# Kernel optimization log

Hardware: AMD Instinct MI355X
Metric: run time of the kernel (lower is better)

The kernel has to match this reference:

```python
import jax, jax.numpy as jnp
import numpy as np

# WAGE-style quantizer (NeuroSim training path): round to 2^(b-1) levels, clip to (-1+1/S, 1-1/S),
# straight-through estimator for gradients.

def wage_q(x, bits=8):
    S = 2.0 ** (bits - 1)
    q = jnp.clip(jnp.round(x * S) / S, -1.0 + 1.0 / S, 1.0 - 1.0 / S)
    return x + jax.lax.stop_gradient(q - x)


def qconv(x, w, stride, pad, wl_w=8, wl_a=8):
    wq = wage_q(w, wl_w)
    y = jax.lax.conv_general_dilated(
        x, wq, window_strides=(stride, stride),
        padding=[(pad, pad), (pad, pad)],
        dimension_numbers=('NCHW', 'OIHW', 'NCHW'))
    return wage_q(y, wl_a)


def pad_hw(x, p):
    return jnp.pad(x, ((0, 0), (0, 0), (p, p), (p, p)))


def crop_like(x, tgt):
    return x[:, :, :tgt.shape[2], :tgt.shape[3]]


WEIGHT_SHAPES = {
    'w1': (64, 4, 3, 3), 'w2': (128, 64, 3, 3), 'w3': (256, 128, 3, 3), 'w4': (512, 256, 3, 3),
    'wr11': (512, 512, 3, 3), 'wr12': (512, 512, 3, 3), 'wr21': (512, 512, 3, 3), 'wr22': (512, 512, 3, 3),
    'wd3': (128, 512, 4, 4), 'wd2': (64, 416, 4, 4), 'wd1': (4, 224, 4, 4),
    'wu43': (32, 512, 4, 4), 'wu32': (32, 416, 4, 4), 'wu21': (32, 224, 4, 4), 'wu10': (32, 100, 4, 4),
    'wfc': (1, 32),
}


def setup_inputs() -> dict:
    key = jax.random.key(0)
    keys = jax.random.split(key, len(WEIGHT_SHAPES) + 1)
    inp = {'x': jax.random.normal(keys[0], (8, 4, 256, 256), dtype=jnp.float32)}
    for i, (name, shp) in enumerate(WEIGHT_SHAPES.items()):
        fan_in = int(np.prod(shp[1:]))
        inp[name] = jax.random.normal(keys[i + 1], shp, dtype=jnp.float32) / np.sqrt(fan_in)
    return inp


def reference(x, w1, w2, w3, w4, wr11, wr12, wr21, wr22,
              wd3, wd2, wd1, wu43, wu32, wu21, wu10, wfc):
    c1 = qconv(x, w1, 2, 1)        # [B,64,128,128]
    c2 = qconv(c1, w2, 2, 1)       # [B,128,64,64]
    c3 = qconv(c2, w3, 2, 1)       # [B,256,32,32]
    c4 = qconv(c3, w4, 2, 1)       # [B,512,16,16]
    r11 = qconv(c4, wr11, 1, 1)
    r12 = (1.0 - qconv(r11, wr12, 1, 1)) * c4
    r21 = qconv(r12, wr21, 1, 1)
    r22 = (1.0 - qconv(r21, wr22, 1, 1)) * r12
    r22p = pad_hw(r22, 8)                                   # [B,512,32,32]
    flow4_up = crop_like(qconv(r22p, wu43, 1, 2), c3)       # [B,32,32,32]
    d3 = crop_like(qconv(r22p, wd3, 1, 2), c3)              # [B,128,32,32]
    cat3 = pad_hw(jnp.concatenate([c3, d3, flow4_up], 1), 16)  # [B,416,64,64]
    flow3_up = crop_like(qconv(cat3, wu32, 1, 2), c2)
    d2 = crop_like(qconv(cat3, wd2, 1, 2), c2)
    cat2 = pad_hw(jnp.concatenate([c2, d2, flow3_up], 1), 32)  # [B,224,128,128]
    flow2_up = crop_like(qconv(cat2, wu21, 1, 2), c1)
    d1 = crop_like(qconv(cat2, wd1, 1, 2), c1)
    cat1 = pad_hw(jnp.concatenate([c1, d1, flow2_up], 1), 64)  # [B,100,256,256]
    u10 = qconv(cat1, wu10, 1, 2)                              # [B,32,257,257]
    feat = jnp.max(u10, axis=(2, 3))                           # AdaptiveMaxPool2d((1,1))
    out = wage_q(feat @ wage_q(wfc, 8).T, 8)                   # QLinear 32->1
    return out
```

## Files before the change

### kernel.cpp

```cpp
#include <hip/hip_runtime.h>

#define DEV __device__ __forceinline__

typedef __attribute__((ext_vector_type(4))) int i32x4;

DEV int wqi(float y) {
    int q = (int)rintf(y * 128.0f);
    return q < -127 ? -127 : (q > 127 ? 127 : q);
}
DEV unsigned encf(float f) { unsigned u = __float_as_uint(f); return (u & 0x80000000u) ? ~u : (u | 0x80000000u); }
DEV float decf(unsigned u) { return (u & 0x80000000u) ? __uint_as_float(u ^ 0x80000000u) : __uint_as_float(~u); }
DEV float wq8f(float x) {
    float q = rintf(x * 128.0f) * 0.0078125f;
    return fminf(fmaxf(q, -0.9921875f), 0.9921875f);
}

#define GLOAD16(g, l) __builtin_amdgcn_global_load_lds( \
    (const __attribute__((address_space(1))) void*)(g), \
    (__attribute__((address_space(3))) void*)(l), 16, 0, 0)

struct PackDesc {
    const float* w0; const float* w1; uint4* dst;
    int OC0, OC1, CinW, K, noct, nch64u, ndup, gsz;
};
struct PackArgs { PackDesc d[11]; int bofs[12]; };

__global__ void __launch_bounds__(256) k_packall(PackArgs a) {
    __shared__ unsigned char sb[16 * (64 * 16 + 4)];
    const int b = blockIdx.x;
    int i = 0;
    #pragma unroll
    for (int j = 1; j < 11; ++j) if (b >= a.bofs[j]) i = j;
    const PackDesc D = a.d[i];
    const int b2 = b - a.bofs[i];
    const int oct = b2 % D.noct;
    const int ch64u = b2 / D.noct;
    const int K2 = D.K * D.K;
    const int NCHT = D.nch64u * D.ndup;
    const int row_elems = 64 * K2;
    const int SSTR = row_elems + 4;
    const int QR = row_elems / 4;
    const int NQ = 16 * QR;
    const int cin0 = ch64u * 64;
    const int tid = threadIdx.x;
    const int og = oct / D.gsz, ol = oct % D.gsz;

    for (int q = tid; q < NQ; q += 256) {
        const int r = q / QR, j = q - r * QR;
        const int oc = oct * 16 + r;
        const float* src = nullptr; int oci = 0;
        if (oc < D.OC0) { src = D.w0; oci = oc; }
        else if (oc < D.OC0 + D.OC1) { src = D.w1; oci = oc - D.OC0; }
        const int e0 = j * 4;
        float v[4] = {0.f, 0.f, 0.f, 0.f};
        if (src != nullptr) {
            const float* p = src + ((size_t)oci * D.CinW + cin0) * K2 + e0;
            const int cin_last = cin0 + (e0 + 3) / K2;
            if (cin_last < D.CinW) {
                const float4 f4 = *(const float4*)p;
                v[0] = f4.x; v[1] = f4.y; v[2] = f4.z; v[3] = f4.w;
            } else {
                #pragma unroll
                for (int e = 0; e < 4; ++e) {
                    const int cin = cin0 + (e0 + e) / K2;
                    if (cin < D.CinW) v[e] = p[e];
                }
            }
        }
        unsigned pk = 0;
        #pragma unroll
        for (int e = 0; e < 4; ++e) pk |= ((unsigned)(wqi(v[e]) & 255)) << (e * 8);
        *(unsigned*)&sb[r * SSTR + e0] = pk;
    }
    __syncthreads();

    const int outN = K2 * 64;
    for (int idx = tid; idx < outN; idx += 256) {
        const int kpos = idx >> 6, lane = idx & 63;
        const int l15 = lane & 15, g = lane >> 4;
        unsigned wd[4] = {0u, 0u, 0u, 0u};
        #pragma unroll
        for (int e = 0; e < 16; ++e) {
            const unsigned bval = sb[l15 * SSTR + (g * 16 + e) * K2 + kpos];
            wd[e >> 2] |= bval << ((e & 3) * 8);
        }
        uint4 u; u.x = wd[0]; u.y = wd[1]; u.z = wd[2]; u.w = wd[3];
        for (int d = 0; d < D.ndup; ++d) {
            const int ch64 = ch64u + d * D.nch64u;
            D.dst[((size_t)((og * NCHT + ch64) * K2 + kpos) * D.gsz + ol) * 64 + lane] = u;
        }
    }
}

__global__ void __launch_bounds__(256) k_conv1(const float* __restrict__ x, const float* __restrict__ w1,
                                               signed char* __restrict__ cat1) {
    __shared__ float sw2[36][64];
    __shared__ float sin_[4][17][17];
    const int tid = threadIdx.x;
    const int n = blockIdx.y;
    const int oh0 = (blockIdx.x >> 4) * 8, ow0 = (blockIdx.x & 15) * 8;
    for (int i = tid; i < 2304; i += 256) sw2[i % 36][i / 36] = wq8f(w1[i]);
    const int ih0 = oh0 * 2 - 1, iw0 = ow0 * 2 - 1;
    for (int i = tid; i < 4 * 289; i += 256) {
        const int c = i / 289, rem = i % 289, r = rem / 17, cc = rem % 17;
        const int ih = ih0 + r, iw = iw0 + cc;
        float v = 0.f;
        if ((unsigned)ih < 256u && (unsigned)iw < 256u) v = x[((size_t)(n * 4 + c) * 256 + ih) * 256 + iw];
        sin_[c][r][cc] = v;
    }
    __syncthreads();
    const int sp = tid & 63, ocg = tid >> 6;
    const int oh = sp >> 3, ow = sp & 7;
    float acc[16];
    #pragma unroll
    for (int j = 0; j < 16; ++j) acc[j] = 0.f;
    #pragma unroll
    for (int c = 0; c < 4; ++c)
    #pragma unroll
    for (int kh = 0; kh < 3; ++kh)
    #pragma unroll
    for (int kw = 0; kw < 3; ++kw) {
        const float v = sin_[c][oh * 2 + kh][ow * 2 + kw];
        const float4* wp4 = (const float4*)&sw2[c * 9 + kh * 3 + kw][ocg * 16];
        #pragma unroll
        for (int q = 0; q < 4; ++q) {
            const float4 wv = wp4[q];
            acc[q * 4 + 0] = fmaf(v, wv.x, acc[q * 4 + 0]);
            acc[q * 4 + 1] = fmaf(v, wv.y, acc[q * 4 + 1]);
            acc[q * 4 + 2] = fmaf(v, wv.z, acc[q * 4 + 2]);
            acc[q * 4 + 3] = fmaf(v, wv.w, acc[q * 4 + 3]);
        }
    }
    const size_t pix = ((size_t)(n * 128) + oh0 + oh) * 128 + ow0 + ow;
    unsigned wd[4] = {0u, 0u, 0u, 0u};
    #pragma unroll
    for (int j = 0; j < 16; ++j)
        wd[j >> 2] |= ((unsigned)(wqi(acc[j]) & 255)) << ((j & 3) * 8);
    uint4 u; u.x = wd[0]; u.y = wd[1]; u.z = wd[2]; u.w = wd[3];
    *(uint4*)(cat1 + pix * 112 + ocg * 16) = u;
}

__global__ void k_init(unsigned* __restrict__ feat, uint4* __restrict__ zbuf) {
    feat[threadIdx.x] = encf(-2.0f);
    if (threadIdx.x < 64) { uint4 z; z.x = z.y = z.z = z.w = 0u; zbuf[threadIdx.x] = z; }
}

__global__ void k_fc(const unsigned* __restrict__ feat, const float* __restrict__ wfc,
                     float* __restrict__ out) {
    int n = threadIdx.x;
    if (n < 8) {
        float s = 0.f;
        for (int c = 0; c < 32; ++c) s += decf(feat[n * 32 + c]) * wq8f(wfc[c]);
        out[n] = wq8f(s);
    }
}

template<int CMODE>
__global__ void __launch_bounds__(256) k_comb(const int* __restrict__ ps, int D, int G,
                                              int NP, int OC, double inv,
                                              signed char* __restrict__ dst, int dstr, int dch,
                                              const void* __restrict__ res, int rstr,
                                              signed char* __restrict__ dhl, int dhlstr,
                                              short* __restrict__ dj) {
    const int t = blockIdx.x * 256 + threadIdx.x;
    const int opc = OC / 4;
    const int total = NP * opc;
    if (t >= total) return;
    const int pix = t / opc, oc0 = (t - pix * opc) * 4;
    const size_t base = (size_t)pix * OC + oc0;
    const size_t NPOC = (size_t)NP * OC;
    long v[4] = {0, 0, 0, 0};
    int sidx = 0;
    for (int d = 0; d < D; ++d) {
        long s0 = 0, s1 = 0, s2 = 0, s3 = 0;
        for (int g = 0; g < G; ++g, ++sidx) {
            const int4 p = *(const int4*)(ps + sidx * NPOC + base);
            s0 += p.x; s1 += p.y; s2 += p.z; s3 += p.w;
        }
        v[0] = v[0] * 256 + s0; v[1] = v[1] * 256 + s1;
        v[2] = v[2] * 256 + s2; v[3] = v[3] * 256 + s3;
    }
    if constexpr (CMODE == 0) {
        unsigned pk = 0;
        #pragma unroll
        for (int j = 0; j < 4; ++j)
            pk |= (unsigned)(wqi((float)((double)v[j] * inv)) & 255) << (j * 8);
        *(unsigned*)(dst + (size_t)pix * dstr + dch + oc0) = pk;
    } else {
        #pragma unroll
        for (int j = 0; j < 4; ++j) {
            const int qi = wqi((float)((double)v[j] * inv));
            const int oc = oc0 + j;
            if constexpr (CMODE == 1) {
                const int rv = (int)((const signed char*)res)[(size_t)pix * rstr + oc];
                const int jj = (128 - qi) * rv;
                const int d0 = ((jj + 128) & 255) - 128;
                const int t1 = (jj - d0) >> 8;
                dhl[(size_t)pix * dhlstr + oc] = (signed char)t1;
                dhl[(size_t)pix * dhlstr + 512 + oc] = (signed char)d0;
                dj[(size_t)pix * 512 + oc] = (short)jj;
            } else {
                const int rv = (int)((const short*)res)[(size_t)pix * rstr + oc];
                const int jj = (128 - qi) * rv;
                const int d0 = ((jj + 128) & 255) - 128;
                const int t1 = (jj - d0) >> 8;
                const int d1 = ((t1 + 128) & 255) - 128;
                const int d2 = (t1 - d1) >> 8;
                dhl[(size_t)pix * dhlstr + oc] = (signed char)d2;
                dhl[(size_t)pix * dhlstr + 512 + oc] = (signed char)d1;
                dhl[(size_t)pix * dhlstr + 1024 + oc] = (signed char)d0;
            }
        }
    }
}

template<int K, int STR, int WM, int WN, int BN, int CHQ, int NBUF, int MODE>
__global__ void __launch_bounds__(256) k_mconv(
    const signed char* __restrict__ s0, int Ctot, int st0,
    int S, int padeff,
    const uint4* __restrict__ wqp, int nchtot,
    signed char* __restrict__ dst, int dstr, int dch,
    unsigned* __restrict__ feat, int* __restrict__ ps,
    const signed char* __restrict__ zbuf,
    int OCv, int OH, int OW, int TILES_W, int nch,
    int NT, int NOCG, int swzq, int ORD)
{
    constexpr int TH = WM * 4;
    constexpr int RH = (TH - 1) * STR + K, RW = 7 * STR + K;
    constexpr int UNITS = CHQ / 16;
    constexpr int UPPS = UNITS + 1;
    constexpr int NKC = CHQ / 64;
    constexpr int K2 = K * K;
    constexpr int NUS = RH * RW * UPPS;
    constexpr int ROUNDS = (NUS + 255) / 256;
    constexpr int NUPS = ROUNDS * 256;
    constexpr int AHEAD = NBUF - 1;
    __shared__ uint4 lds[NBUF * NUPS];
    __shared__ int sred[4][2][16];

    const int tid = threadIdx.x, lane = tid & 63, w = tid >> 6;
    const int wm = w % WM, wn = w / WM;
    const int l15 = lane & 15, g = lane >> 4;

    const int b = blockIdx.x;
    const int work = (b & 7) * swzq + (b >> 3);
    int tile, n, ocg, slice;
    if (ORD == 0) {
        ocg = work % NOCG; const int t2 = work / NOCG;
        tile = t2 % NT; const int t3 = t2 / NT;
        n = t3 & 7; slice = t3 >> 3;
    } else {
        tile = work % NT; const int t2 = work / NT;
        n = t2 & 7; const int t3 = t2 >> 3;
        ocg = t3 % NOCG; slice = t3 / NOCG;
    }
    const int cin_off = slice * nch * CHQ;
    const int group = ocg * WN + wn;

    const int tileh = tile / TILES_W, tilew = tile % TILES_W;
    const int oh0 = tileh * TH, ow0 = tilew * 8;
    const int ih0 = oh0 * STR - padeff, iw0 = ow0 * STR - padeff;
    const int blk_oct0 = ocg * (WN * BN);

    int pixb[2];
    #pragma unroll
    for (int am = 0; am < 2; ++am) {
        const int sp = wm * 32 + am * 16 + l15;
        pixb[am] = ((sp >> 3) * STR) * RW + (sp & 7) * STR;
    }

    int climit[ROUNDS];
    const signed char* gpb[ROUNDS];
    #pragma unroll
    for (int rd = 0; rd < ROUNDS; ++rd) {
        const int d = rd * 256 + tid;
        int cl = -1;
        const signed char* gb = zbuf;
        if (d < NUS) {
            const int pix = d / UPPS;
            const int u = d - pix * UPPS;
            const int r = pix / RW, c = pix - r * RW;
            const int ih = ih0 + r, iw = iw0 + c;
            if (u < UNITS && (unsigned)ih < (unsigned)S && (unsigned)iw < (unsigned)S) {
                cl = Ctot - cin_off - u * 16;
                gb = s0 + (((size_t)n * S + ih) * S + iw) * st0 + cin_off + u * 16;
            }
        }
        climit[rd] = cl; gpb[rd] = gb;
    }

    i32x4 acc[2][BN];
    #pragma unroll
    for (int am = 0; am < 2; ++am)
        #pragma unroll
        for (int bn = 0; bn < BN; ++bn) acc[am][bn] = (i32x4){0, 0, 0, 0};

    auto issue = [&](int ch, int buf) {
        uint4* lb = &lds[buf * NUPS];
        const int chv = ch * CHQ;
        #pragma unroll
        for (int rd = 0; rd < ROUNDS; ++rd) {
            const signed char* gp = (chv < climit[rd]) ? (gpb[rd] + chv) : zbuf;
            GLOAD16(gp, lb + rd * 256 + (tid & ~63));
        }
    };

    #pragma unroll
    for (int i = 0; i < AHEAD; ++i) if (i < nch) issue(i, i % NBUF);

    for (int ch = 0; ch < nch; ++ch) {
        if (ch + AHEAD < nch) issue(ch + AHEAD, (ch + AHEAD) % NBUF);
        const int infl = (nch - 1 - ch < AHEAD) ? nch - 1 - ch : AHEAD;
        if (infl >= 2)      __builtin_amdgcn_s_waitcnt(0xF70 | (2 * ROUNDS));
        else if (infl == 1) __builtin_amdgcn_s_waitcnt(0xF70 | ROUNDS);
        else                __builtin_amdgcn_s_waitcnt(0xF70);
        __builtin_amdgcn_s_barrier();
        __builtin_amdgcn_sched_barrier(0);
        const int bufo = (ch % NBUF) * NUPS;
        const int pb0 = bufo + pixb[0] * UPPS + g;
        const int pb1 = bufo + pixb[1] * UPPS + g;
        const uint4* wrow = wqp + ((size_t)(group * nchtot + (slice * nch + ch) * NKC) * K2 * BN) * 64 + lane;
        #pragma unroll
        for (int kpos = 0; kpos < K2; ++kpos) {
            const int kh = kpos / K, kw = kpos % K;
            const int po = (kh * RW + kw) * UPPS;
            #pragma unroll
            for (int kc = 0; kc < NKC; ++kc) {
                i32x4 bfr[BN];
                #pragma unroll
                for (int bn = 0; bn < BN; ++bn) {
                    union { uint4 u; i32x4 v; } bu;
                    bu.u = wrow[(kc * K2 * BN + kpos * BN + bn) * 64];
                    bfr[bn] = bu.v;
                }
                union { uint4 u; i32x4 v; } a0, a1;
                a0.u = lds[pb0 + po + kc * 4];
                a1.u = lds[pb1 + po + kc * 4];
                #pragma unroll
                for (int bn = 0; bn < BN; ++bn) {
                    acc[0][bn] = __builtin_amdgcn_mfma_i32_16x16x64_i8(a0.v, bfr[bn], acc[0][bn], 0, 0, 0);
                    acc[1][bn] = __builtin_amdgcn_mfma_i32_16x16x64_i8(a1.v, bfr[bn], acc[1][bn], 0, 0, 0);
                }
            }
        }
        __builtin_amdgcn_sched_barrier(0);
        __builtin_amdgcn_s_barrier();
    }

    if constexpr (MODE == 2) {
        #pragma unroll
        for (int bn = 0; bn < BN; ++bn) {
            int m = (int)0x80000000;
            #pragma unroll
            for (int am = 0; am < 2; ++am)
                #pragma unroll
                for (int rg = 0; rg < 4; ++rg) {
                    const int sp = wm * 32 + am * 16 + g * 4 + rg;
                    const int oh = oh0 + (sp >> 3), ow = ow0 + (sp & 7);
                    const int v = acc[am][bn][rg];
                    if (oh < OH && ow < OW && v > m) m = v;
                }
            int o = __shfl_xor(m, 16); if (o > m) m = o;
            o = __shfl_xor(m, 32); if (o > m) m = o;
            if (lane < 16) sred[w][bn][l15] = m;
        }
        __syncthreads();
        if (tid < BN * 16) {
            const int bn = tid >> 4, l = tid & 15;
            int mm = sred[0][bn][l];
            #pragma unroll
            for (int i = 1; i < WM * WN; ++i) { const int o = sred[i][bn][l]; if (o > mm) mm = o; }
            const float y = (float)mm * (1.f / 16384.f);
            const float v = (float)wqi(y) * 0.0078125f;
            atomicMax(&feat[n * 32 + (blk_oct0 + bn) * 16 + l], encf(v));
        }
    } else if constexpr (MODE == 3) {
        #pragma unroll
        for (int am = 0; am < 2; ++am)
        #pragma unroll
        for (int bn = 0; bn < BN; ++bn)
        #pragma unroll
        for (int rg = 0; rg < 4; ++rg) {
            const int sp = wm * 32 + am * 16 + g * 4 + rg;
            const int oh = oh0 + (sp >> 3), ow = ow0 + (sp & 7);
            const int oc = (blk_oct0 + wn * BN + bn) * 16 + l15;
            if (oh < OH && ow < OW && oc < OCv) {
                ps[(((size_t)slice * 8 + n) * OH * OW + (size_t)oh * OW + ow) * OCv + oc] = acc[am][bn][rg];
            }
        }
    } else {
        #pragma unroll
        for (int am = 0; am < 2; ++am)
        #pragma unroll
        for (int bn = 0; bn < BN; ++bn)
        #pragma unroll
        for (int rg = 0; rg < 4; ++rg) {
            const int sp = wm * 32 + am * 16 + g * 4 + rg;
            const int oh = oh0 + (sp >> 3), ow = ow0 + (sp & 7);
            const int oc = (blk_oct0 + wn * BN + bn) * 16 + l15;
            if (oh < OH && ow < OW && oc < OCv) {
                const size_t pixo = (size_t)(n * OH + oh) * OW + ow;
                const float y = (float)acc[am][bn][rg] * (1.f / 16384.f);
                dst[pixo * dstr + dch + oc] = (signed char)wqi(y);
            }
        }
    }
}

extern "C" void kernel_launch(void* const* d_in, const int* in_sizes, int n_in,
                              void* d_out, int out_size, void* d_ws, size_t ws_size,
                              hipStream_t stream)
{
    (void)in_sizes; (void)n_in; (void)out_size; (void)ws_size;
    const float* x = (const float*)d_in[0];
    const float* wfc = (const float*)d_in[16];
    float* out = (float*)d_out;

    char* ws = (char*)d_ws;
    size_t off = 0;
    auto alloc = [&](size_t bytes) { char* p = ws + off; off += (bytes + 255) & ~(size_t)255; return p; };

    struct PH { int i0, OC0, i1, OC1, CinW, K, noct, nch64u, ndup, gsz; };
    static const PH ph[11] = {
        {2, 128, -1, 0,  64, 3,  8, 1, 1, 2},
        {3, 256, -1, 0, 128, 3, 16, 2, 1, 2},
        {4, 512, -1, 0, 256, 3, 32, 4, 1, 2},
        {5, 512, -1, 0, 512, 3, 32, 8, 1, 2},
        {6, 512, -1, 0, 512, 3, 32, 8, 1, 2},
        {7, 512, -1, 0, 512, 3, 32, 8, 2, 2},
        {8, 512, -1, 0, 512, 3, 32, 8, 1, 2},
        {9, 128, 12, 32, 512, 4, 10, 8, 3, 2},
        {10, 64, 13, 32, 416, 4,  6, 7, 1, 2},
        {11,  4, 14, 32, 224, 4,  3, 4, 1, 3},
        {15, 32, -1, 0, 100, 4,  2, 2, 1, 2}};

    PackArgs pa;
    int bacc = 0;
    uint4* wp[11];
    for (int i = 0; i < 11; ++i) {
        const int nch64 = ph[i].nch64u * ph[i].ndup;
        const int nel = nch64 * ph[i].K * ph[i].K * ph[i].noct * 64;
        wp[i] = (uint4*)alloc((size_t)nel * 16);
        pa.d[i].w0 = (const float*)d_in[ph[i].i0];
        pa.d[i].w1 = (ph[i].i1 >= 0) ? (const float*)d_in[ph[i].i1] : nullptr;
        pa.d[i].dst = wp[i];
        pa.d[i].OC0 = ph[i].OC0; pa.d[i].OC1 = ph[i].OC1;
        pa.d[i].CinW = ph[i].CinW; pa.d[i].K = ph[i].K; pa.d[i].noct = ph[i].noct;
        pa.d[i].nch64u = ph[i].nch64u; pa.d[i].ndup = ph[i].ndup;
        pa.d[i].gsz = ph[i].gsz;
        pa.bofs[i] = bacc;
        bacc += ph[i].noct * ph[i].nch64u;
    }
    pa.bofs[11] = bacc;

    signed char* cat1b = (signed char*)alloc((size_t)8*128*128*112);
    signed char* cat2b = (signed char*)alloc((size_t)8*64*64*224);
    signed char* cat3b = (signed char*)alloc((size_t)8*32*32*416);
    signed char* c4b   = (signed char*)alloc((size_t)8*16*16*512);
    signed char* r11b  = (signed char*)alloc((size_t)8*16*16*512);
    signed char* r12d  = (signed char*)alloc((size_t)8*16*16*1024);
    short*       r12j  = (short*)alloc((size_t)8*16*16*512 * 2);
    signed char* r22d  = (signed char*)alloc((size_t)8*16*16*1536);
    int*         psum  = (int*)alloc((size_t)4*8*16*16*512 * 4);
    unsigned*    featb = (unsigned*)alloc(256 * 4);
    uint4*       zbuf  = (uint4*)alloc(1024);

    k_packall<<<dim3((unsigned)bacc), dim3(256), 0, stream>>>(pa);
    k_init<<<dim3(1), dim3(256), 0, stream>>>(featb, zbuf);
    k_conv1<<<dim3(256, 8), dim3(256), 0, stream>>>(x, (const float*)d_in[1], cat1b);

    const signed char* zb = (const signed char*)zbuf;
    const void* nv = nullptr;

    k_mconv<3,2,2,2,2,64,1,0><<<dim3(1024), 256, 0, stream>>>(
        cat1b,64,112, 128,1, wp[0],1, cat2b,224,0, nullptr,nullptr, zb,
        128,64,64,8, 1, 64,2,128, 0);
    k_mconv<3,2,2,2,2,64,2,0><<<dim3(512), 256, 0, stream>>>(
        cat2b,128,224, 64,1, wp[1],2, cat3b,416,0, nullptr,nullptr, zb,
        256,32,32,4, 2, 16,4,64, 0);
    k_mconv<3,2,2,2,2,64,1,3><<<dim3(1024), 256, 0, stream>>>(
        cat3b,256,416, 32,1, wp[2],4, nullptr,0,0, nullptr,(int*)psum, zb,
        512,16,16,2, 1, 4,8,128, 1);
    k_comb<0><<<dim3(1024), 256, 0, stream>>>(psum,1,4, 2048,512, 1.0/16384.0, c4b,512,0, nv,0, nullptr,0,nullptr);
    k_mconv<3,1,4,1,2,128,1,3><<<dim3(1024), 256, 0, stream>>>(
        c4b,512,512, 16,1, wp[3],8, nullptr,0,0, nullptr,psum, zb,
        512,16,16,2, 1, 2,16,128, 1);
    k_comb<0><<<dim3(1024), 256, 0, stream>>>(psum,1,4, 2048,512, 1.0/16384.0, r11b,512,0, nv,0, nullptr,0,nullptr);
    k_mconv<3,1,4,1,2,64,3,3><<<dim3(512), 256, 0, stream>>>(
        r11b,512,512, 16,1, wp[4],8, nullptr,0,0, nullptr,psum, zb,
        512,16,16,2, 4, 2,16,64, 1);
    k_comb<1><<<dim3(1024), 256, 0, stream>>>(psum,1,2, 2048,512, 1.0/16384.0, nullptr,0,0, c4b,512, r12d,1024,r12j);
    k_mconv<3,1,4,1,2,64,2,3><<<dim3(1024), 256, 0, stream>>>(
        r12d,1024,1024, 16,1, wp[5],16, nullptr,0,0, nullptr,psum, zb,
        512,16,16,2, 4, 2,16,128, 1);
    k_comb<0><<<dim3(1024), 256, 0, stream>>>(psum,2,2, 2048,512, 1.0/2097152.0, r11b,512,0, nv,0, nullptr,0,nullptr);
    k_mconv<3,1,4,1,2,64,3,3><<<dim3(512), 256, 0, stream>>>(
        r11b,512,512, 16,1, wp[6],8, nullptr,0,0, nullptr,psum, zb,
        512,16,16,2, 4, 2,16,64, 1);
    k_comb<2><<<dim3(1024), 256, 0, stream>>>(psum,1,2, 2048,512, 1.0/16384.0, nullptr,0,0, r12j,512, r22d,1536,nullptr);
    k_mconv<4,1,4,1,2,64,2,3><<<dim3(960), 256, 0, stream>>>(
        r22d,1536,1536, 16,10, wp[7],24, nullptr,0,0, nullptr,psum, zb,
        160,32,32,4, 8, 8,5,120, 1);
    k_comb<0><<<dim3(1280), 256, 0, stream>>>(psum,3,1, 8192,160, 1.0/268435456.0, cat3b,416,256, nv,0, nullptr,0,nullptr);
    k_mconv<4,1,4,1,2,64,2,0><<<dim3(768), 256, 0, stream>>>(
        cat3b,416,416, 32,18, wp[8],7, cat2b,224,128, nullptr,nullptr, zb,
        96,64,64,8, 7, 32,3,96, 0);
    k_mconv<4,1,4,1,3,64,2,0><<<dim3(1024), 256, 0, stream>>>(
        cat2b,224,224, 64,34, wp[9],4, cat1b,112,64, nullptr,nullptr, zb,
        48,128,128,16, 4, 128,1,128, 0);
    k_mconv<4,1,4,1,2,128,1,2><<<dim3(4488), 256, 0, stream>>>(
        cat1b,112,112, 128,66, wp[10],2, nullptr,0,0, featb,nullptr, zb,
        32,257,257,33, 1, 561,1,561, 0);
    k_fc<<<dim3(1), dim3(64), 0, stream>>>(featb, wfc, out);
}
```

Measured before the change: 329.4 us.

## Skip decoder conv tiles whose receptive field lies entirely in zero padding

The decoder stages pad their inputs heavily (8, 16, 32 and 64 pixels), so large border regions of each output can only be convolutions of zeros. Those outputs quantize to exactly zero. The change launches the four decoder convs only over the central output window, using new row and column offsets in the conv kernel and an output-region guard in the combine kernel. The skipped channel ranges of the concat buffers are pre-zeroed with a new fill kernel, and the max-pool accumulator now starts at 0, since the padded region guarantees zeros are part of the max. This removes most of the redundant MMA work, especially in the final 100-channel 257x257 conv, at the cost of three small fill launches and bounds that must exactly match the padding geometry.

```diff
diff --git a/kernel.cpp b/kernel.cpp
--- a/kernel.cpp
+++ b/kernel.cpp
@@ -92,6 +92,15 @@
     }
 }
 
+__global__ void __launch_bounds__(256) k_zfill(uint4* __restrict__ p, int npix, int stride_u4,
+                                               int off_u4, int cnt, int total) {
+    const int idx = blockIdx.x * 256 + threadIdx.x;
+    if (idx >= total) return;
+    const int pix = idx / cnt, j = idx - pix * cnt;
+    uint4 z; z.x = z.y = z.z = z.w = 0u;
+    p[(size_t)pix * stride_u4 + off_u4 + j] = z;
+}
+
 __global__ void __launch_bounds__(256) k_conv1(const float* __restrict__ x, const float* __restrict__ w1,
                                                signed char* __restrict__ cat1) {
     __shared__ float sw2[36][64];
@@ -141,7 +150,7 @@
 }
 
 __global__ void k_init(unsigned* __restrict__ feat, uint4* __restrict__ zbuf) {
-    feat[threadIdx.x] = encf(-2.0f);
+    feat[threadIdx.x] = encf(0.0f);
     if (threadIdx.x < 64) { uint4 z; z.x = z.y = z.z = z.w = 0u; zbuf[threadIdx.x] = z; }
 }
 
@@ -161,12 +170,16 @@
                                               signed char* __restrict__ dst, int dstr, int dch,
                                               const void* __restrict__ res, int rstr,
                                               signed char* __restrict__ dhl, int dhlstr,
-                                              short* __restrict__ dj) {
+                                              short* __restrict__ dj,
+                                              int ohw, int OWW, int r0, int r1, int c0, int c1) {
     const int t = blockIdx.x * 256 + threadIdx.x;
     const int opc = OC / 4;
     const int total = NP * opc;
     if (t >= total) return;
     const int pix = t / opc, oc0 = (t - pix * opc) * 4;
+    const int sp = pix % ohw;
+    const int oh = sp / OWW, ow = sp - oh * OWW;
+    if (oh < r0 || oh > r1 || ow < c0 || ow > c1) return;
     const size_t base = (size_t)pix * OC + oc0;
     const size_t NPOC = (size_t)NP * OC;
     long v[4] = {0, 0, 0, 0};
@@ -223,7 +236,7 @@
     unsigned* __restrict__ feat, int* __restrict__ ps,
     const signed char* __restrict__ zbuf,
     int OCv, int OH, int OW, int TILES_W, int nch,
-    int NT, int NOCG, int swzq, int ORD)
+    int NT, int NOCG, int swzq, int ORD, int ohb, int owb)
 {
     constexpr int TH = WM * 4;
     constexpr int RH = (TH - 1) * STR + K, RW = 7 * STR + K;
@@ -258,7 +271,7 @@
     const int group = ocg * WN + wn;
 
     const int tileh = tile / TILES_W, tilew = tile % TILES_W;
-    const int oh0 = tileh * TH, ow0 = tilew * 8;
+    const int oh0 = ohb + tileh * TH, ow0 = owb + tilew * 8;
     const int ih0 = oh0 * STR - padeff, iw0 = ow0 * STR - padeff;
     const int blk_oct0 = ocg * (WN * BN);
 
@@ -467,49 +480,59 @@
 
     k_packall<<<dim3((unsigned)bacc), dim3(256), 0, stream>>>(pa);
     k_init<<<dim3(1), dim3(256), 0, stream>>>(featb, zbuf);
+    k_zfill<<<dim3((131072*3 + 255)/256), 256, 0, stream>>>((uint4*)cat1b, 131072, 7, 4, 3, 131072*3);
+    k_zfill<<<dim3((32768*6 + 255)/256), 256, 0, stream>>>((uint4*)cat2b, 32768, 14, 8, 6, 32768*6);
+    k_zfill<<<dim3((8192*10 + 255)/256), 256, 0, stream>>>((uint4*)cat3b, 8192, 26, 16, 10, 8192*10);
     k_conv1<<<dim3(256, 8), dim3(256), 0, stream>>>(x, (const float*)d_in[1], cat1b);
 
     const signed char* zb = (const signed char*)zbuf;
     const void* nv = nullptr;
+    const int BIG = 1 << 30;
 
     k_mconv<3,2,2,2,2,64,1,0><<<dim3(1024), 256, 0, stream>>>(
         cat1b,64,112, 128,1, wp[0],1, cat2b,224,0, nullptr,nullptr, zb,
-        128,64,64,8, 1, 64,2,128, 0);
+        128,64,64,8, 1, 64,2,128, 0, 0,0);
     k_mconv<3,2,2,2,2,64,2,0><<<dim3(512), 256, 0, stream>>>(
         cat2b,128,224, 64,1, wp[1],2, cat3b,416,0, nullptr,nullptr, zb,
-        256,32,32,4, 2, 16,4,64, 0);
+        256,32,32,4, 2, 16,4,64, 0, 0,0);
     k_mconv<3,2,2,2,2,64,1,3><<<dim3(1024), 256, 0, stream>>>(
         cat3b,256,416, 32,1, wp[2],4, nullptr,0,0, nullptr,(int*)psum, zb,
-        512,16,16,2, 1, 4,8,128, 1);
-    k_comb<0><<<dim3(1024), 256, 0, stream>>>(psum,1,4, 2048,512, 1.0/16384.0, c4b,512,0, nv,0, nullptr,0,nullptr);
+        512,16,16,2, 1, 4,8,128, 1, 0,0);
+    k_comb<0><<<dim3(1024), 256, 0, stream>>>(psum,1,4, 2048,512, 1.0/16384.0, c4b,512,0, nv,0, nullptr,0,nullptr,
+        256,16, 0,BIG,0,BIG);
     k_mconv<3,1,4,1,2,128,1,3><<<dim3(1024), 256, 0, stream>>>(
         c4b,512,512, 16,1, wp[3],8, nullptr,0,0, nullptr,psum, zb,
-        512,16,16,2, 1, 2,16,128, 1);
-    k_comb<0><<<dim3(1024), 256, 0, stream>>>(psum,1,4, 2048,512, 1.0/16384.0, r11b,512,0, nv,0, nullptr,0,nullptr);
+        512,16,16,2, 1, 2,16,128, 1, 0,0);
+    k_comb<0><<<dim3(1024), 256, 0, stream>>>(psum,1,4, 2048,512, 1.0/16384.0, r11b,512,0, nv,0, nullptr,0,nullptr,
+        256,16, 0,BIG,0,BIG);
     k_mconv<3,1,4,1,2,64,3,3><<<dim3(512), 256, 0, stream>>>(
         r11b,512,512, 16,1, wp[4],8, nullptr,0,0, nullptr,psum, zb,
-        512,16,16,2, 4, 2,16,64, 1);
-    k_comb<1><<<dim3(1024), 256, 0, stream>>>(psum,1,2, 2048,512, 1.0/16384.0, nullptr,0,0, c4b,512, r12d,1024,r12j);
+        512,16,16,2, 4, 2,16,64, 1, 0,0);
+    k_comb<1><<<dim3(1024), 256, 0, stream>>>(psum,1,2, 2048,512, 1.0/16384.0, nullptr,0,0, c4b,512, r12d,1024,r12j,
+        256,16, 0,BIG,0,BIG);
     k_mconv<3,1,4,1,2,64,2,3><<<dim3(1024), 256, 0, stream>>>(
         r12d,1024,1024, 16,1, wp[5],16, nullptr,0,0, nullptr,psum, zb,
-        512,16,16,2, 4, 2,16,128, 1);
-    k_comb<0><<<dim3(1024), 256, 0, stream>>>(psum,2,2, 2048,512, 1.0/2097152.0, r11b,512,0, nv,0, nullptr,0,nullptr);
+        512,16,16,2, 4, 2,16,128, 1, 0,0);
+    k_comb<0><<<dim3(1024), 256, 0, stream>>>(psum,2,2, 2048,512, 1.0/2097152.0, r11b,512,0, nv,0, nullptr,0,nullptr,
+        256,16, 0,BIG,0,BIG);
     k_mconv<3,1,4,1,2,64,3,3><<<dim3(512), 256, 0, stream>>>(
         r11b,512,512, 16,1, wp[6],8, nullptr,0,0, nullptr,psum, zb,
-        512,16,16,2, 4, 2,16,64, 1);
-    k_comb<2><<<dim3(1024), 256, 0, stream>>>(psum,1,2, 2048,512, 1.0/16384.0, nullptr,0,0, r12j,512, r22d,1536,nullptr);
-    k_mconv<4,1,4,1,2,64,2,3><<<dim3(960), 256, 0, stream>>>(
+        512,16,16,2, 4, 2,16,64, 1, 0,0);
+    k_comb<2><<<dim3(1024), 256, 0, stream>>>(psum,1,2, 2048,512, 1.0/16384.0, nullptr,0,0, r12j,512, r22d,1536,nullptr,
+        256,16, 0,BIG,0,BIG);
+    k_mconv<4,1,4,1,2,64,2,3><<<dim3(720), 256, 0, stream>>>(
         r22d,1536,1536, 16,10, wp[7],24, nullptr,0,0, nullptr,psum, zb,
-        160,32,32,4, 8, 8,5,120, 1);
-    k_comb<0><<<dim3(1280), 256, 0, stream>>>(psum,3,1, 8192,160, 1.0/268435456.0, cat3b,416,256, nv,0, nullptr,0,nullptr);
-    k_mconv<4,1,4,1,2,64,2,0><<<dim3(768), 256, 0, stream>>>(
+        160,32,32,3, 8, 6,5,90, 1, 7,7);
+    k_comb<0><<<dim3(1280), 256, 0, stream>>>(psum,3,1, 8192,160, 1.0/268435456.0, cat3b,416,256, nv,0, nullptr,0,nullptr,
+        1024,32, 7,25,7,25);
+    k_mconv<4,1,4,1,2,64,2,0><<<dim3(360), 256, 0, stream>>>(
         cat3b,416,416, 32,18, wp[8],7, cat2b,224,128, nullptr,nullptr, zb,
-        96,64,64,8, 7, 32,3,96, 0);
-    k_mconv<4,1,4,1,3,64,2,0><<<dim3(1024), 256, 0, stream>>>(
+        96,64,64,5, 7, 15,3,45, 0, 15,15);
+    k_mconv<4,1,4,1,3,64,2,0><<<dim3(360), 256, 0, stream>>>(
         cat2b,224,224, 64,34, wp[9],4, cat1b,112,64, nullptr,nullptr, zb,
-        48,128,128,16, 4, 128,1,128, 0);
-    k_mconv<4,1,4,1,2,128,1,2><<<dim3(4488), 256, 0, stream>>>(
+        48,128,128,9, 4, 45,1,45, 0, 31,31);
+    k_mconv<4,1,4,1,2,128,1,2><<<dim3(1224), 256, 0, stream>>>(
         cat1b,112,112, 128,66, wp[10],2, nullptr,0,0, featb,nullptr, zb,
-        32,257,257,33, 1, 561,1,561, 0);
+        32,257,257,17, 1, 153,1,153, 0, 63,63);
     k_fc<<<dim3(1), dim3(64), 0, stream>>>(featb, wfc, out);
 }
```

Measured after the change: 298.1 us. 1.1x faster.
